# Kernel optimization log

Measured on AMD Instinct MI355X. Metric: run time of the kernel, lower is better.

## Reference

```python
import jax, jax.numpy as jnp
from jax import lax
import numpy as np

N, F_IN, D_MODEL = 8192, 128, 256
D_INNER, D_STATE, D_CONV, DT_RANK = 512, 16, 4, 16  # expand=2, d_state=16, d_conv=4, dt_rank=ceil(256/16)
BN_EPS = 1e-5


def setup_inputs() -> dict:
    key = jax.random.key(0)
    ks = jax.random.split(key, 12)
    rn = lambda k, s, sc: jax.random.normal(k, s, jnp.float32) * sc
    x = rn(ks[0], (N, F_IN), 1.0)
    # normalized dense adjacency (row sums ~1)
    adj = jax.random.uniform(ks[1], (N, N), jnp.float32) * (2.0 / N)
    w_gcn = rn(ks[2], (F_IN, D_MODEL), 1.0 / np.sqrt(F_IN))
    b_gcn = rn(ks[3], (D_MODEL,), 0.02)
    bn_gamma = jnp.ones((D_MODEL,), jnp.float32)
    bn_beta = jnp.zeros((D_MODEL,), jnp.float32)
    w_in = rn(ks[4], (2 * D_INNER, D_MODEL), 1.0 / np.sqrt(D_MODEL))
    conv_w = rn(ks[5], (D_INNER, D_CONV), 1.0 / np.sqrt(D_CONV))
    conv_b = rn(ks[6], (D_INNER,), 0.02)
    w_xproj = rn(ks[7], (DT_RANK + 2 * D_STATE, D_INNER), 1.0 / np.sqrt(D_INNER))
    w_dt = rn(ks[8], (D_INNER, DT_RANK), 1.0 / np.sqrt(DT_RANK))
    b_dt = rn(ks[9], (D_INNER,), 0.1)
    A_log = jnp.log(jnp.broadcast_to(jnp.arange(1, D_STATE + 1, dtype=jnp.float32), (D_INNER, D_STATE)))
    D_skip = jnp.ones((D_INNER,), jnp.float32)
    w_out = rn(ks[10], (D_MODEL, D_INNER), 1.0 / np.sqrt(D_INNER))
    return dict(x=x, adj=adj, w_gcn=w_gcn, b_gcn=b_gcn, bn_gamma=bn_gamma, bn_beta=bn_beta,
                w_in=w_in, conv_w=conv_w, conv_b=conv_b, w_xproj=w_xproj, w_dt=w_dt,
                b_dt=b_dt, A_log=A_log, D_skip=D_skip, w_out=w_out)


def _forward(x, adj, w_gcn, b_gcn, bn_gamma, bn_beta, w_in, conv_w, conv_b,
             w_xproj, w_dt, b_dt, A_log, D_skip, w_out):
    # --- GCN layer: adj @ (x @ W) + b ---
    h = adj @ (x @ w_gcn) + b_gcn            # (N, D_MODEL)
    h = jax.nn.relu(h)
    # dropout: eval mode -> identity
    # --- BatchNorm1d (batch statistics, biased var, as torch training norm) ---
    mean = jnp.mean(h, axis=0)
    var = jnp.var(h, axis=0)
    h = (h - mean) * lax.rsqrt(var + BN_EPS) * bn_gamma + bn_beta  # (N, D_MODEL)

    # --- Mamba block, batch=1, seq_len=N ---
    xz = h @ w_in.T                          # (N, 2*D_INNER)
    xm, z = jnp.split(xz, 2, axis=-1)        # (N, D_INNER) each

    # causal depthwise conv1d (kernel D_CONV) + SiLU
    xp = jnp.pad(xm, ((D_CONV - 1, 0), (0, 0)))
    xc = conv_b + sum(xp[i:i + N] * conv_w[:, i] for i in range(D_CONV))  # (N, D_INNER)
    xc = jax.nn.silu(xc)

    # input-dependent SSM parameters
    x_dbl = xc @ w_xproj.T                   # (N, DT_RANK + 2*D_STATE)
    dt_r = x_dbl[:, :DT_RANK]
    B = x_dbl[:, DT_RANK:DT_RANK + D_STATE]  # (N, D_STATE)
    C = x_dbl[:, DT_RANK + D_STATE:]         # (N, D_STATE)
    dt = jax.nn.softplus(dt_r @ w_dt.T + b_dt)  # (N, D_INNER)

    A = -jnp.exp(A_log)                      # (D_INNER, D_STATE)
    deltaA = jnp.exp(dt[:, :, None] * A[None])                 # (N, D_INNER, D_STATE)
    deltaBu = dt[:, :, None] * B[:, None, :] * xc[:, :, None]  # (N, D_INNER, D_STATE)

    def step(hs, inp):
        dA, dBu, c = inp
        hs = dA * hs + dBu                   # (D_INNER, D_STATE)
        return hs, hs @ c                    # emit (D_INNER,)

    h0 = jnp.zeros((D_INNER, D_STATE), xc.dtype)
    _, ys = lax.scan(step, h0, (deltaA, deltaBu, C))  # ys: (N, D_INNER)

    y = ys + D_skip * xc
    y = y * jax.nn.silu(z)
    out_m = y @ w_out.T                      # (N, D_MODEL)
    return out_m + h                         # residual


def reference(x, adj, w_gcn, b_gcn, bn_gamma, bn_beta, w_in, conv_w, conv_b,
              w_xproj, w_dt, b_dt, A_log, D_skip, w_out):
    return _forward(x, adj, w_gcn, b_gcn, bn_gamma, bn_beta, w_in, conv_w, conv_b,
                    w_xproj, w_dt, b_dt, A_log, D_skip, w_out)
```

## Files before the change

kernel.cpp:

```cpp
#include <hip/hip_runtime.h>
#include <stdint.h>

#define NN   8192
#define FIN  128
#define DM   256
#define DI   512
#define DST  16
#define NC   256
#define CL   32

typedef short bf16x8 __attribute__((ext_vector_type(8)));
typedef float f32x4 __attribute__((ext_vector_type(4)));
union FragU { unsigned u[4]; uint4 u4; bf16x8 v; };

__device__ __forceinline__ unsigned short f2bf(float x){
  unsigned u = __float_as_uint(x);
  return (unsigned short)((u + 0x7FFFu + ((u >> 16) & 1u)) >> 16);
}
__device__ __forceinline__ unsigned pack2(float a, float b){
  return (unsigned)f2bf(a) | ((unsigned)f2bf(b) << 16);
}
__device__ __forceinline__ unsigned pack2rn(float a, float b){
  unsigned ua = __float_as_uint(a) + 0x8000u;
  unsigned ub = __float_as_uint(b) + 0x8000u;
  return __builtin_amdgcn_perm(ub, ua, 0x07060302u);
}
__device__ __forceinline__ float bf2f(unsigned short u){
  return __uint_as_float(((unsigned)u) << 16);
}
__device__ __forceinline__ float sigmoidf_(float x){ return 1.f / (1.f + __expf(-x)); }
__device__ __forceinline__ f32x4 zero4(){ f32x4 z; z[0]=0.f; z[1]=0.f; z[2]=0.f; z[3]=0.f; return z; }

#define ASYNC16(g, l) __builtin_amdgcn_global_load_lds( \
    (const __attribute__((address_space(1))) void*)(g), \
    (__attribute__((address_space(3))) void*)(l), 16, 0, 0)
#define WAITVM10 asm volatile("s_waitcnt vmcnt(10)" ::: "memory")
#define WAITVM0  asm volatile("s_waitcnt vmcnt(0)" ::: "memory")
#define WAITLGKM0 asm volatile("s_waitcnt lgkmcnt(0)" ::: "memory")
#define BARRIER  asm volatile("s_barrier" ::: "memory")

constexpr size_t OFF_XWT   = 0;
constexpr size_t OFF_HB    = OFF_XWT   + (size_t)DM*NN*2;
constexpr size_t OFF_HBNB  = OFF_HB    + (size_t)NN*DM*2;
constexpr size_t OFF_WINB  = OFF_HBNB  + (size_t)NN*DM*2;
constexpr size_t OFF_WXPB  = OFF_WINB  + (size_t)1024*256*2;
constexpr size_t OFF_WOUTB = OFF_WXPB  + (size_t)48*512*2;
constexpr size_t OFF_XMB   = OFF_WOUTB + (size_t)256*512*2;
constexpr size_t OFF_ZB    = OFF_XMB   + (size_t)NN*DI*2;
constexpr size_t OFF_XCB   = OFF_ZB    + (size_t)NN*DI*2;
constexpr size_t OFF_XDBL  = OFF_XCB   + (size_t)NN*DI*2;
constexpr size_t OFF_DT    = OFF_XDBL  + (size_t)NN*48*4;
constexpr size_t OFF_PF    = OFF_DT    + (size_t)NN*DI*4;
constexpr size_t OFF_CY    = OFF_PF    + (size_t)NC*DI*DST*8;
constexpr size_t OFF_YB    = OFF_CY    + (size_t)NC*DI*DST*4;
constexpr size_t OFF_BNS   = OFF_YB    + (size_t)NN*DI*2;
constexpr size_t OFF_BNS2  = OFF_BNS   + 256*4;
constexpr size_t WS_NEED   = OFF_BNS2  + 256*4;
constexpr size_t OFF_HP    = OFF_PF;

__global__ __launch_bounds__(256) void prep_kernel(
    const float* __restrict__ w_in, const float* __restrict__ w_xp, const float* __restrict__ w_out,
    unsigned short* __restrict__ o_in, unsigned short* __restrict__ o_xp, unsigned short* __restrict__ o_out)
{
  int i = blockIdx.x * 256 + threadIdx.x;
  if (i < 1024*256) o_in[i]  = f2bf(w_in[i]);
  if (i < 48*512)   o_xp[i]  = f2bf(w_xp[i]);
  if (i < 256*512)  o_out[i] = f2bf(w_out[i]);
}

__global__ __launch_bounds__(256) void gemm1_kernel(
    const float* __restrict__ x, const float* __restrict__ w, unsigned short* __restrict__ xwT)
{
  __shared__ float xs[16*128];
  const int t = threadIdx.x;
  const int m0 = blockIdx.x * 16;
  {
    int r = t >> 4, c0 = (t & 15) * 8;
    const float* src = x + (size_t)(m0 + r)*FIN + c0;
    *(float4*)&xs[r*128 + c0]     = *(const float4*)src;
    *(float4*)&xs[r*128 + c0 + 4] = *(const float4*)(src + 4);
  }
  __syncthreads();
  const int n = t;
  float acc[16];
  #pragma unroll
  for (int m = 0; m < 16; ++m) acc[m] = 0.f;
  for (int k = 0; k < 128; k += 4){
    float w0 = w[(size_t)k*DM + n];
    float w1 = w[(size_t)(k+1)*DM + n];
    float w2 = w[(size_t)(k+2)*DM + n];
    float w3 = w[(size_t)(k+3)*DM + n];
    #pragma unroll
    for (int m = 0; m < 16; ++m){
      float4 xv = *(const float4*)&xs[m*128 + k];
      acc[m] = fmaf(xv.x, w0, acc[m]);
      acc[m] = fmaf(xv.y, w1, acc[m]);
      acc[m] = fmaf(xv.z, w2, acc[m]);
      acc[m] = fmaf(xv.w, w3, acc[m]);
    }
  }
  unsigned outp[8];
  #pragma unroll
  for (int m = 0; m < 8; ++m) outp[m] = pack2(acc[2*m], acc[2*m+1]);
  unsigned short* dst = xwT + (size_t)n*NN + m0;
  ((uint4*)dst)[0] = *(uint4*)&outp[0];
  ((uint4*)dst)[1] = *(uint4*)&outp[4];
}

__global__ __launch_bounds__(256, 2) void gemm2_kernel(
    const float* __restrict__ adj, const unsigned short* __restrict__ xwT,
    float* __restrict__ hp)
{
  extern __shared__ char lds[];
  const int t = threadIdx.x;
  const int wave = t >> 6, lane = t & 63, r = lane & 15, q = lane >> 4;
  const int mt = (int)blockIdx.x >> 2, ks = (int)blockIdx.x & 3;
  const int m0 = mt * 32;
  const int kb = ks * 2048;

  const float* asrc[2];
  #pragma unroll
  for (int j = 0; j < 2; ++j){
    int si = t + 256*j;
    int row = si >> 4, d = si & 15;
    int g = (d - 3*row) & 15;
    asrc[j] = adj + (size_t)(m0 + row)*NN + kb + g*4;
  }
  const unsigned short* bsrc[8];
  #pragma unroll
  for (int j = 0; j < 8; ++j){
    int si = t + 256*j;
    int n = si >> 3, d = si & 7;
    int g = (d - 3*n) & 7;
    bsrc[j] = xwT + (size_t)n*NN + kb + g*8;
  }

  f32x4 acc[2][4];
  #pragma unroll
  for (int mi = 0; mi < 2; ++mi)
    #pragma unroll
    for (int ni = 0; ni < 4; ++ni) acc[mi][ni] = zero4();

  #pragma unroll
  for (int s = 0; s < 2; ++s){
    char* L = lds + s*40960;
    int k0 = s*64;
    ASYNC16(asrc[0] + k0, L + t*16);
    ASYNC16(asrc[1] + k0, L + (t + 256)*16);
    #pragma unroll
    for (int j = 0; j < 8; ++j)
      ASYNC16(bsrc[j] + k0, L + 8192 + (t + 256*j)*16);
  }

  int aoffF[2][2][2];
  int boffU[2][4];
  #pragma unroll
  for (int ks2 = 0; ks2 < 2; ++ks2){
    #pragma unroll
    for (int mi = 0; mi < 2; ++mi){
      int m = mi*16 + r;
      int g0 = ks2*8 + 2*q;
      aoffF[ks2][mi][0] = m*64 + (((g0    ) + 3*m) & 15)*4;
      aoffF[ks2][mi][1] = m*64 + (((g0 + 1) + 3*m) & 15)*4;
    }
    #pragma unroll
    for (int ni = 0; ni < 4; ++ni){
      int n = wave*64 + ni*16 + r;
      int g = ks2*4 + q;
      boffU[ks2][ni] = 512 + n*8 + ((g + 3*n) & 7);
    }
  }

  for (int k = 0; k < 32; ++k){
    if (k < 31) { WAITVM10; } else { WAITVM0; }
    BARRIER;
    char* Lb = lds + (k & 1)*40960;
    const float* Af = (const float*)Lb;
    const uint4* Bu = (const uint4*)Lb;
    float4 pa[2][2][2];
    FragU fb[2][4];
    #pragma unroll
    for (int ks2 = 0; ks2 < 2; ++ks2){
      #pragma unroll
      for (int mi = 0; mi < 2; ++mi){
        pa[ks2][mi][0] = *(const float4*)(Af + aoffF[ks2][mi][0]);
        pa[ks2][mi][1] = *(const float4*)(Af + aoffF[ks2][mi][1]);
      }
      #pragma unroll
      for (int ni = 0; ni < 4; ++ni) fb[ks2][ni].u4 = Bu[boffU[ks2][ni]];
    }
    WAITLGKM0;
    BARRIER;
    if (k < 30){
      int k0 = (k + 2) * 64;
      ASYNC16(asrc[0] + k0, Lb + t*16);
      ASYNC16(asrc[1] + k0, Lb + (t + 256)*16);
      #pragma unroll
      for (int j = 0; j < 8; ++j)
        ASYNC16(bsrc[j] + k0, Lb + 8192 + (t + 256*j)*16);
    }
    FragU fa[2][2];
    #pragma unroll
    for (int ks2 = 0; ks2 < 2; ++ks2)
      #pragma unroll
      for (int mi = 0; mi < 2; ++mi){
        fa[ks2][mi].u[0] = pack2rn(pa[ks2][mi][0].x, pa[ks2][mi][0].y);
        fa[ks2][mi].u[1] = pack2rn(pa[ks2][mi][0].z, pa[ks2][mi][0].w);
        fa[ks2][mi].u[2] = pack2rn(pa[ks2][mi][1].x, pa[ks2][mi][1].y);
        fa[ks2][mi].u[3] = pack2rn(pa[ks2][mi][1].z, pa[ks2][mi][1].w);
      }
    #pragma unroll
    for (int ks2 = 0; ks2 < 2; ++ks2)
      #pragma unroll
      for (int mi = 0; mi < 2; ++mi)
        #pragma unroll
        for (int ni = 0; ni < 4; ++ni)
          acc[mi][ni] = __builtin_amdgcn_mfma_f32_16x16x32_bf16(fa[ks2][mi].v, fb[ks2][ni].v, acc[mi][ni], 0, 0, 0);
  }

  float* hpo = hp + (size_t)ks * ((size_t)NN * DM);
  #pragma unroll
  for (int mi = 0; mi < 2; ++mi)
    #pragma unroll
    for (int ni = 0; ni < 4; ++ni){
      const int n = wave*64 + ni*16 + r;
      #pragma unroll
      for (int jr = 0; jr < 4; ++jr){
        const int m = m0 + mi*16 + q*4 + jr;
        hpo[(size_t)m*DM + n] = acc[mi][ni][jr];
      }
    }
}

__global__ __launch_bounds__(256) void hred_kernel(
    const float* __restrict__ hp, const float* __restrict__ b_gcn,
    unsigned short* __restrict__ hb, float* __restrict__ bns, float* __restrict__ bns2)
{
  const size_t NND = (size_t)NN * DM;
  const int c = threadIdx.x;
  const int m0 = blockIdx.x * 32;
  const float bias = b_gcn[c];
  float s1 = 0.f, s2 = 0.f;
  #pragma unroll 8
  for (int rr = 0; rr < 32; ++rr){
    size_t idx = (size_t)(m0 + rr)*DM + c;
    float v = hp[idx] + hp[NND + idx] + hp[2*NND + idx] + hp[3*NND + idx] + bias;
    v = fmaxf(v, 0.f);
    hb[idx] = f2bf(v);
    s1 += v; s2 += v*v;
  }
  atomicAdd(bns + c, s1);
  atomicAdd(bns2 + c, s2);
}

__global__ __launch_bounds__(256) void bnapply_kernel(
    const unsigned short* __restrict__ hb, const float* __restrict__ s1, const float* __restrict__ s2,
    const float* __restrict__ gamma, const float* __restrict__ beta,
    unsigned short* __restrict__ hbnb)
{
  int base = (blockIdx.x*256 + threadIdx.x) * 2;
  int c0 = base & (DM - 1);
  ushort2 hv = *(const ushort2*)(hb + base);
  float mA = s1[c0] * (1.f/NN),   mB = s1[c0+1] * (1.f/NN);
  float vA = s2[c0] * (1.f/NN) - mA*mA, vB = s2[c0+1] * (1.f/NN) - mB*mB;
  float iA = rsqrtf(vA + 1e-5f), iB = rsqrtf(vB + 1e-5f);
  float a = (bf2f(hv.x) - mA)*iA*gamma[c0]   + beta[c0];
  float b = (bf2f(hv.y) - mB)*iB*gamma[c0+1] + beta[c0+1];
  ushort2 o; o.x = f2bf(a); o.y = f2bf(b);
  *(ushort2*)(hbnb + base) = o;
}

__global__ __launch_bounds__(256) void gemm3_kernel(
    const unsigned short* __restrict__ Ab, const unsigned short* __restrict__ Wb,
    unsigned short* __restrict__ xmb, unsigned short* __restrict__ zb)
{
  __shared__ uint4 alds[2048];
  const int t = threadIdx.x;
  const int wave = t >> 6, lane = t & 63, r = lane & 15, q = lane >> 4;
  const int mb = ((int)blockIdx.x & 127) * 64;
  const int nb = ((int)blockIdx.x >> 7) * 128;
  const int wm = wave & 1, wn = wave >> 1;

  #pragma unroll
  for (int j = 0; j < 8; ++j){
    int si = j*256 + t;
    int row = si >> 5, dg = si & 31;
    int sg = dg ^ (row & 31);
    ASYNC16(Ab + (size_t)(mb + row)*DM + sg*8, (char*)alds + si*16);
  }
  __syncthreads();

  f32x4 acc[2][4];
  #pragma unroll
  for (int mi = 0; mi < 2; ++mi)
    #pragma unroll
    for (int ni = 0; ni < 4; ++ni) acc[mi][ni] = zero4();

  const unsigned short* bp[4];
  #pragma unroll
  for (int ni = 0; ni < 4; ++ni)
    bp[ni] = Wb + (size_t)(nb + wn*64 + ni*16 + r)*DM + q*8;
  FragU fb[4];
  #pragma unroll
  for (int ni = 0; ni < 4; ++ni) fb[ni].u4 = *(const uint4*)bp[ni];

  #pragma unroll
  for (int it = 0; it < 8; ++it){
    FragU fbn[4];
    if (it < 7){
      #pragma unroll
      for (int ni = 0; ni < 4; ++ni) fbn[ni].u4 = *(const uint4*)(bp[ni] + (it+1)*32);
    }
    FragU fa[2];
    #pragma unroll
    for (int mi = 0; mi < 2; ++mi){
      int row = wm*32 + mi*16 + r;
      int g = it*4 + q;
      fa[mi].u4 = alds[row*32 + (g ^ (row & 31))];
    }
    #pragma unroll
    for (int mi = 0; mi < 2; ++mi)
      #pragma unroll
      for (int ni = 0; ni < 4; ++ni)
        acc[mi][ni] = __builtin_amdgcn_mfma_f32_16x16x32_bf16(fa[mi].v, fb[ni].v, acc[mi][ni], 0, 0, 0);
    if (it < 7){
      #pragma unroll
      for (int ni = 0; ni < 4; ++ni) fb[ni] = fbn[ni];
    }
  }
  #pragma unroll
  for (int mi = 0; mi < 2; ++mi)
    #pragma unroll
    for (int ni = 0; ni < 4; ++ni){
      int nc = nb + wn*64 + ni*16 + r;
      unsigned short* dst = (nc < 512) ? (xmb + nc) : (zb + (nc - 512));
      #pragma unroll
      for (int jr = 0; jr < 4; ++jr){
        int m = mb + wm*32 + mi*16 + q*4 + jr;
        dst[(size_t)m*DI] = f2bf(acc[mi][ni][jr]);
      }
    }
}

__global__ __launch_bounds__(256) void conv_kernel(
    const unsigned short* __restrict__ xmb, const float* __restrict__ conv_w, const float* __restrict__ conv_b,
    unsigned short* __restrict__ xcb)
{
  const int d0 = threadIdx.x * 2;
  const int n0 = blockIdx.x * 32;
  float4 wa = *(const float4*)(conv_w + (size_t)d0*4);
  float4 wb = *(const float4*)(conv_w + (size_t)d0*4 + 4);
  float2 bias = *(const float2*)(conv_b + d0);
  float x0a=0.f,x1a=0.f,x2a=0.f, x0b=0.f,x1b=0.f,x2b=0.f;
  #pragma unroll
  for (int j = 0; j < 3; ++j){
    int n = n0 - 3 + j;
    float va = 0.f, vb = 0.f;
    if (n >= 0){
      ushort2 u = *(const ushort2*)(xmb + (size_t)n*DI + d0);
      va = bf2f(u.x); vb = bf2f(u.y);
    }
    if (j == 0){ x0a = va; x0b = vb; }
    else if (j == 1){ x1a = va; x1b = vb; }
    else { x2a = va; x2b = vb; }
  }
  for (int j = 0; j < 32; ++j){
    int n = n0 + j;
    ushort2 u = *(const ushort2*)(xmb + (size_t)n*DI + d0);
    float x3a = bf2f(u.x), x3b = bf2f(u.y);
    float sa = bias.x + wa.x*x0a + wa.y*x1a + wa.z*x2a + wa.w*x3a;
    float sb = bias.y + wb.x*x0b + wb.y*x1b + wb.z*x2b + wb.w*x3b;
    float va = sa * sigmoidf_(sa);
    float vb = sb * sigmoidf_(sb);
    ushort2 o; o.x = f2bf(va); o.y = f2bf(vb);
    *(ushort2*)(xcb + (size_t)n*DI + d0) = o;
    x0a=x1a; x1a=x2a; x2a=x3a;
    x0b=x1b; x1b=x2b; x2b=x3b;
  }
}

__global__ __launch_bounds__(256) void gemm4_kernel(
    const unsigned short* __restrict__ Ab, const unsigned short* __restrict__ Wb, float* __restrict__ xdbl)
{
  __shared__ uint4 alds[2048];
  const int t = threadIdx.x;
  const int wave = t >> 6, lane = t & 63, r = lane & 15, q = lane >> 4;
  const int m0 = (int)blockIdx.x * 32;
  #pragma unroll
  for (int j = 0; j < 8; ++j){
    int si = j*256 + t;
    int row = si >> 6, dg = si & 63;
    int sg = dg ^ (row & 31);
    ASYNC16(Ab + (size_t)(m0 + row)*DI + sg*8, (char*)alds + si*16);
  }
  __syncthreads();
  f32x4 acc[2][3];
  #pragma unroll
  for (int mi = 0; mi < 2; ++mi)
    #pragma unroll
    for (int ni = 0; ni < 3; ++ni) acc[mi][ni] = zero4();
  const int kq = wave * 128;
  const unsigned short* bp[3];
  #pragma unroll
  for (int ni = 0; ni < 3; ++ni) bp[ni] = Wb + (size_t)(ni*16 + r)*DI + kq + q*8;
  FragU fb[3];
  #pragma unroll
  for (int ni = 0; ni < 3; ++ni) fb[ni].u4 = *(const uint4*)bp[ni];
  #pragma unroll
  for (int it = 0; it < 4; ++it){
    FragU fbn[3];
    if (it < 3){
      #pragma unroll
      for (int ni = 0; ni < 3; ++ni) fbn[ni].u4 = *(const uint4*)(bp[ni] + (it+1)*32);
    }
    FragU fa[2];
    #pragma unroll
    for (int mi = 0; mi < 2; ++mi){
      int row = mi*16 + r;
      int g = (kq >> 3) + it*4 + q;
      fa[mi].u4 = alds[row*64 + (g ^ (row & 31))];
    }
    #pragma unroll
    for (int mi = 0; mi < 2; ++mi)
      #pragma unroll
      for (int ni = 0; ni < 3; ++ni)
        acc[mi][ni] = __builtin_amdgcn_mfma_f32_16x16x32_bf16(fa[mi].v, fb[ni].v, acc[mi][ni], 0, 0, 0);
    if (it < 3){
      #pragma unroll
      for (int ni = 0; ni < 3; ++ni) fb[ni] = fbn[ni];
    }
  }
  __syncthreads();
  float* red = (float*)alds;
  if (wave > 0){
    int base = ((wave - 1)*64 + lane)*24;
    #pragma unroll
    for (int mi = 0; mi < 2; ++mi)
      #pragma unroll
      for (int ni = 0; ni < 3; ++ni)
        #pragma unroll
        for (int jr = 0; jr < 4; ++jr)
          red[base + (mi*3 + ni)*4 + jr] = acc[mi][ni][jr];
  }
  __syncthreads();
  if (wave == 0){
    #pragma unroll
    for (int w = 0; w < 3; ++w){
      int base = (w*64 + lane)*24;
      #pragma unroll
      for (int mi = 0; mi < 2; ++mi)
        #pragma unroll
        for (int ni = 0; ni < 3; ++ni)
          #pragma unroll
          for (int jr = 0; jr < 4; ++jr)
            acc[mi][ni][jr] += red[base + (mi*3 + ni)*4 + jr];
    }
    #pragma unroll
    for (int mi = 0; mi < 2; ++mi)
      #pragma unroll
      for (int ni = 0; ni < 3; ++ni)
        #pragma unroll
        for (int jr = 0; jr < 4; ++jr)
          xdbl[(size_t)(m0 + mi*16 + q*4 + jr)*48 + ni*16 + r] = acc[ni >= 0 ? mi : mi][ni][jr];
  }
}

__global__ __launch_bounds__(256) void dt_kernel(
    const float* __restrict__ xdbl, const float* __restrict__ w_dt, const float* __restrict__ b_dt,
    float* __restrict__ dt)
{
  __shared__ float xr[64*16];
  const int t = threadIdx.x;
  const int dg = (int)blockIdx.x & 1;
  const int n0 = ((int)blockIdx.x >> 1) * 64;
  const int d = dg*256 + t;
  #pragma unroll
  for (int j = 0; j < 4; ++j){
    int idx = t + 256*j;
    xr[idx] = xdbl[(size_t)(n0 + (idx >> 4))*48 + (idx & 15)];
  }
  __syncthreads();
  const float4* wp = (const float4*)(w_dt + (size_t)d*16);
  float4 w0 = wp[0], w1 = wp[1], w2 = wp[2], w3 = wp[3];
  float bias = b_dt[d];
  for (int j = 0; j < 64; ++j){
    const float4* xp = (const float4*)(xr + j*16);
    float4 a0 = xp[0], a1 = xp[1], a2 = xp[2], a3 = xp[3];
    float a = bias;
    a += w0.x*a0.x + w0.y*a0.y + w0.z*a0.z + w0.w*a0.w;
    a += w1.x*a1.x + w1.y*a1.y + w1.z*a1.z + w1.w*a1.w;
    a += w2.x*a2.x + w2.y*a2.y + w2.z*a2.z + w2.w*a2.w;
    a += w3.x*a3.x + w3.y*a3.y + w3.z*a3.z + w3.w*a3.w;
    float o = (a > 20.f) ? a : log1pf(__expf(a));
    dt[(size_t)(n0 + j)*DI + d] = o;
  }
}

__global__ __launch_bounds__(256) void scanA_kernel(
    const float* __restrict__ dt, const unsigned short* __restrict__ xcb,
    const float* __restrict__ xdbl, const float* __restrict__ A_log,
    float2* __restrict__ PF)
{
  __shared__ float Bs[CL*DST];
  const int t = threadIdx.x;
  const int c = (int)blockIdx.x >> 1;
  const int d = (((int)blockIdx.x & 1) << 8) + t;
  #pragma unroll
  for (int j = 0; j < 2; ++j){
    int idx = t + 256*j;
    Bs[idx] = xdbl[(size_t)(c*CL + (idx >> 4))*48 + 16 + (idx & 15)];
  }
  __syncthreads();
  float Av[DST], hs[DST];
  {
    const float4* Ap = (const float4*)(A_log + (size_t)d*DST);
    #pragma unroll
    for (int s4 = 0; s4 < 4; ++s4){
      float4 a4 = Ap[s4];
      Av[s4*4+0] = -__expf(a4.x); Av[s4*4+1] = -__expf(a4.y);
      Av[s4*4+2] = -__expf(a4.z); Av[s4*4+3] = -__expf(a4.w);
    }
  }
  #pragma unroll
  for (int s = 0; s < DST; ++s) hs[s] = 0.f;
  float sdt = 0.f;
  const size_t rb = (size_t)c*CL*DI + d;
  float dtv = dt[rb], xcv = bf2f(xcb[rb]);
  for (int tt = 0; tt < CL; ++tt){
    float dtn = 0.f, xcn = 0.f;
    if (tt + 1 < CL){
      dtn = dt[rb + (size_t)(tt+1)*DI];
      xcn = bf2f(xcb[rb + (size_t)(tt+1)*DI]);
    }
    float u = dtv * xcv;
    sdt += dtv;
    float bv[DST];
    *(float4*)&bv[0]  = *(const float4*)&Bs[tt*16];
    *(float4*)&bv[4]  = *(const float4*)&Bs[tt*16 + 4];
    *(float4*)&bv[8]  = *(const float4*)&Bs[tt*16 + 8];
    *(float4*)&bv[12] = *(const float4*)&Bs[tt*16 + 12];
    #pragma unroll
    for (int s = 0; s < DST; ++s)
      hs[s] = __expf(dtv * Av[s]) * hs[s] + u * bv[s];
    dtv = dtn; xcv = xcn;
  }
  float4* out = (float4*)(PF + (size_t)c*(DI*DST) + (size_t)d*DST);
  #pragma unroll
  for (int j = 0; j < 8; ++j){
    float4 v;
    v.x = __expf(Av[2*j] * sdt);   v.y = hs[2*j];
    v.z = __expf(Av[2*j+1] * sdt); v.w = hs[2*j+1];
    out[j] = v;
  }
}

__global__ __launch_bounds__(128) void scanB_kernel(
    const float2* __restrict__ PF, float* __restrict__ Cy)
{
  const int ds = (int)blockIdx.x*128 + (int)threadIdx.x;
  float2 A0[16], A1[16];
  #pragma unroll
  for (int j = 0; j < 16; ++j) A0[j] = PF[(size_t)j*8192 + ds];
  #pragma unroll
  for (int j = 0; j < 16; ++j) A1[j] = PF[(size_t)(16 + j)*8192 + ds];
  float cy = 0.f;
  Cy[ds] = 0.f;
  #pragma unroll
  for (int g = 0; g < 16; ++g){
    #pragma unroll
    for (int j = 0; j < 16; ++j){
      int i = g*16 + j;
      if (i < NC - 1){
        float2 pf = (g & 1) ? A1[j] : A0[j];
        cy = pf.x * cy + pf.y;
        Cy[(size_t)(i + 1)*8192 + ds] = cy;
      }
    }
    int gn = g + 2;
    if (gn < 16){
      #pragma unroll
      for (int j = 0; j < 16; ++j){
        float2 v = PF[(size_t)(gn*16 + j)*8192 + ds];
        if (g & 1) A1[j] = v; else A0[j] = v;
      }
    }
  }
}

__global__ __launch_bounds__(256) void scanC_kernel(
    const float* __restrict__ dt, const unsigned short* __restrict__ xcb,
    const float* __restrict__ xdbl, const float* __restrict__ A_log,
    const float* __restrict__ Cy, const float* __restrict__ Dskip,
    const unsigned short* __restrict__ zb, unsigned short* __restrict__ yb)
{
  __shared__ float Bs[CL*DST];
  __shared__ float Cs[CL*DST];
  const int t = threadIdx.x;
  const int c = (int)blockIdx.x >> 1;
  const int d = (((int)blockIdx.x & 1) << 8) + t;
  #pragma unroll
  for (int j = 0; j < 2; ++j){
    int idx = t + 256*j;
    int tg = c*CL + (idx >> 4);
    Bs[idx] = xdbl[(size_t)tg*48 + 16 + (idx & 15)];
    Cs[idx] = xdbl[(size_t)tg*48 + 32 + (idx & 15)];
  }
  __syncthreads();
  float Av[DST], hs[DST];
  {
    const float4* Ap = (const float4*)(A_log + (size_t)d*DST);
    #pragma unroll
    for (int s4 = 0; s4 < 4; ++s4){
      float4 a4 = Ap[s4];
      Av[s4*4+0] = -__expf(a4.x); Av[s4*4+1] = -__expf(a4.y);
      Av[s4*4+2] = -__expf(a4.z); Av[s4*4+3] = -__expf(a4.w);
    }
  }
  {
    const float4* hp4 = (const float4*)(Cy + (size_t)c*(DI*DST) + (size_t)d*DST);
    #pragma unroll
    for (int s4 = 0; s4 < 4; ++s4){
      float4 h4 = hp4[s4];
      hs[s4*4+0] = h4.x; hs[s4*4+1] = h4.y; hs[s4*4+2] = h4.z; hs[s4*4+3] = h4.w;
    }
  }
  const float Dv = Dskip[d];
  const size_t rb = (size_t)c*CL*DI + d;
  float dtv = dt[rb], xcv = bf2f(xcb[rb]);
  unsigned short zv0 = zb[rb];
  for (int tt = 0; tt < CL; ++tt){
    float dtn = 0.f, xcn = 0.f;
    unsigned short zn = 0;
    if (tt + 1 < CL){
      dtn = dt[rb + (size_t)(tt+1)*DI];
      xcn = bf2f(xcb[rb + (size_t)(tt+1)*DI]);
      zn  = zb[rb + (size_t)(tt+1)*DI];
    }
    float u = dtv * xcv;
    float bv[DST], cv[DST];
    *(float4*)&bv[0]  = *(const float4*)&Bs[tt*16];
    *(float4*)&bv[4]  = *(const float4*)&Bs[tt*16 + 4];
    *(float4*)&bv[8]  = *(const float4*)&Bs[tt*16 + 8];
    *(float4*)&bv[12] = *(const float4*)&Bs[tt*16 + 12];
    *(float4*)&cv[0]  = *(const float4*)&Cs[tt*16];
    *(float4*)&cv[4]  = *(const float4*)&Cs[tt*16 + 4];
    *(float4*)&cv[8]  = *(const float4*)&Cs[tt*16 + 8];
    *(float4*)&cv[12] = *(const float4*)&Cs[tt*16 + 12];
    float y0 = 0.f, y1 = 0.f;
    #pragma unroll
    for (int s = 0; s < DST; s += 2){
      hs[s]   = __expf(dtv * Av[s])   * hs[s]   + u * bv[s];
      hs[s+1] = __expf(dtv * Av[s+1]) * hs[s+1] + u * bv[s+1];
      y0 += hs[s]   * cv[s];
      y1 += hs[s+1] * cv[s+1];
    }
    float z = bf2f(zv0);
    float yf = ((y0 + y1) + Dv * xcv) * (z * sigmoidf_(z));
    yb[rb + (size_t)tt*DI] = f2bf(yf);
    dtv = dtn; xcv = xcn; zv0 = zn;
  }
}

__global__ __launch_bounds__(512) void gemm5_kernel(
    const unsigned short* __restrict__ yb, const unsigned short* __restrict__ Wb,
    const unsigned short* __restrict__ hbnb, float* __restrict__ out)
{
  __shared__ uint4 alds[2048];
  const int t = threadIdx.x;
  const int wave = t >> 6, lane = t & 63, r = lane & 15, q = lane >> 4;
  const int m0 = (int)blockIdx.x * 32;
  #pragma unroll
  for (int j = 0; j < 4; ++j){
    int si = j*512 + t;
    int row = si >> 6, dg = si & 63;
    int sg = dg ^ (row & 31);
    ASYNC16(yb + (size_t)(m0 + row)*DI + sg*8, (char*)alds + si*16);
  }
  __syncthreads();
  f32x4 acc[2][2];
  #pragma unroll
  for (int mi = 0; mi < 2; ++mi)
    #pragma unroll
    for (int ni = 0; ni < 2; ++ni) acc[mi][ni] = zero4();
  const int nw = wave * 32;
  const unsigned short* bp0 = Wb + (size_t)(nw + r)*DI + q*8;
  const unsigned short* bp1 = Wb + (size_t)(nw + 16 + r)*DI + q*8;
  FragU fb0, fb1;
  fb0.u4 = *(const uint4*)bp0;
  fb1.u4 = *(const uint4*)bp1;
  #pragma unroll
  for (int it = 0; it < 16; ++it){
    FragU fn0, fn1;
    if (it < 15){
      fn0.u4 = *(const uint4*)(bp0 + (it+1)*32);
      fn1.u4 = *(const uint4*)(bp1 + (it+1)*32);
    }
    FragU fa[2];
    #pragma unroll
    for (int mi = 0; mi < 2; ++mi){
      int row = mi*16 + r;
      int g = it*4 + q;
      fa[mi].u4 = alds[row*64 + (g ^ (row & 31))];
    }
    acc[0][0] = __builtin_amdgcn_mfma_f32_16x16x32_bf16(fa[0].v, fb0.v, acc[0][0], 0, 0, 0);
    acc[0][1] = __builtin_amdgcn_mfma_f32_16x16x32_bf16(fa[0].v, fb1.v, acc[0][1], 0, 0, 0);
    acc[1][0] = __builtin_amdgcn_mfma_f32_16x16x32_bf16(fa[1].v, fb0.v, acc[1][0], 0, 0, 0);
    acc[1][1] = __builtin_amdgcn_mfma_f32_16x16x32_bf16(fa[1].v, fb1.v, acc[1][1], 0, 0, 0);
    if (it < 15){ fb0 = fn0; fb1 = fn1; }
  }
  #pragma unroll
  for (int mi = 0; mi < 2; ++mi)
    #pragma unroll
    for (int ni = 0; ni < 2; ++ni){
      const int n = nw + ni*16 + r;
      #pragma unroll
      for (int jr = 0; jr < 4; ++jr){
        const int m = m0 + mi*16 + q*4 + jr;
        size_t idx = (size_t)m*DM + n;
        out[idx] = acc[mi][ni][jr] + bf2f(hbnb[idx]);
      }
    }
}

extern "C" void kernel_launch(void* const* d_in, const int* in_sizes, int n_in,
                              void* d_out, int out_size, void* d_ws, size_t ws_size,
                              hipStream_t stream)
{
  const float* x      = (const float*)d_in[0];
  const float* adj    = (const float*)d_in[1];
  const float* w_gcn  = (const float*)d_in[2];
  const float* b_gcn  = (const float*)d_in[3];
  const float* gamma  = (const float*)d_in[4];
  const float* beta   = (const float*)d_in[5];
  const float* w_in   = (const float*)d_in[6];
  const float* conv_w = (const float*)d_in[7];
  const float* conv_b = (const float*)d_in[8];
  const float* w_xp   = (const float*)d_in[9];
  const float* w_dt   = (const float*)d_in[10];
  const float* b_dt   = (const float*)d_in[11];
  const float* A_log  = (const float*)d_in[12];
  const float* D_skip = (const float*)d_in[13];
  const float* w_out  = (const float*)d_in[14];
  float* out = (float*)d_out;
  char* ws = (char*)d_ws;
  if (ws_size < WS_NEED) return;

  unsigned short* xwT   = (unsigned short*)(ws + OFF_XWT);
  float*          hp    = (float*)(ws + OFF_HP);
  unsigned short* hb    = (unsigned short*)(ws + OFF_HB);
  unsigned short* hbnb  = (unsigned short*)(ws + OFF_HBNB);
  unsigned short* winb  = (unsigned short*)(ws + OFF_WINB);
  unsigned short* wxpb  = (unsigned short*)(ws + OFF_WXPB);
  unsigned short* woutb = (unsigned short*)(ws + OFF_WOUTB);
  unsigned short* xmb   = (unsigned short*)(ws + OFF_XMB);
  unsigned short* zb    = (unsigned short*)(ws + OFF_ZB);
  unsigned short* xcb   = (unsigned short*)(ws + OFF_XCB);
  float*          xdbl  = (float*)(ws + OFF_XDBL);
  float*          dtb   = (float*)(ws + OFF_DT);
  float2*         PF    = (float2*)(ws + OFF_PF);
  float*          Cy    = (float*)(ws + OFF_CY);
  unsigned short* yb    = (unsigned short*)(ws + OFF_YB);
  float*          bns   = (float*)(ws + OFF_BNS);
  float*          bns2  = (float*)(ws + OFF_BNS2);

  hipMemsetAsync(bns, 0, 2*256*sizeof(float), stream);

  hipFuncSetAttribute((const void*)gemm2_kernel,
                      hipFuncAttributeMaxDynamicSharedMemorySize, 81920);

  prep_kernel   <<<1024, 256, 0, stream>>>(w_in, w_xp, w_out, winb, wxpb, woutb);
  gemm1_kernel  <<<512,  256, 0, stream>>>(x, w_gcn, xwT);
  gemm2_kernel  <<<1024, 256, 81920, stream>>>(adj, xwT, hp);
  hred_kernel   <<<256,  256, 0, stream>>>(hp, b_gcn, hb, bns, bns2);
  bnapply_kernel<<<4096, 256, 0, stream>>>(hb, bns, bns2, gamma, beta, hbnb);
  gemm3_kernel  <<<1024, 256, 0, stream>>>(hbnb, winb, xmb, zb);
  conv_kernel   <<<256,  256, 0, stream>>>(xmb, conv_w, conv_b, xcb);
  gemm4_kernel  <<<256,  256, 0, stream>>>(xcb, wxpb, xdbl);
  dt_kernel     <<<256,  256, 0, stream>>>(xdbl, w_dt, b_dt, dtb);
  scanA_kernel  <<<512,  256, 0, stream>>>(dtb, xcb, xdbl, A_log, PF);
  scanB_kernel  <<<64,   128, 0, stream>>>(PF, Cy);
  scanC_kernel  <<<512,  256, 0, stream>>>(dtb, xcb, xdbl, A_log, Cy, D_skip, zb, yb);
  gemm5_kernel  <<<256,  512, 0, stream>>>(yb, woutb, hbnb, out);
}
```

Measured before the change: 601.9 us.

## Retile adjacency GEMM with register prefetch, bf16 LDS, and fuse dt into gemm4

The adj@XW GEMM moves to 512-thread blocks with 64-row tiles and a 2-way K split instead of 32-row tiles and a 4-way split. That halves the partial-sum traffic that hred has to reduce. A tiles are now loaded into registers, converted to bf16 once, and written to a swizzled LDS layout, replacing async fp32 global-to-LDS copies that every wave had to convert itself. The dt projection plus softplus is fused into the gemm4 epilogue, which removes one kernel launch and a reread of xdbl. The risks are lower occupancy, since there is one 512-thread block per CU with only 256 blocks, and loads that no longer run asynchronously into LDS.

New measurement: 719.3 us. +19.5%, slower.

```diff
diff --git a/kernel.cpp b/kernel.cpp
--- a/kernel.cpp
+++ b/kernel.cpp
@@ -25,6 +25,12 @@
   unsigned ub = __float_as_uint(b) + 0x8000u;
   return __builtin_amdgcn_perm(ub, ua, 0x07060302u);
 }
+__device__ __forceinline__ uint4 packA8(float4 a, float4 b){
+  uint4 w;
+  w.x = pack2rn(a.x, a.y); w.y = pack2rn(a.z, a.w);
+  w.z = pack2rn(b.x, b.y); w.w = pack2rn(b.z, b.w);
+  return w;
+}
 __device__ __forceinline__ float bf2f(unsigned short u){
   return __uint_as_float(((unsigned)u) << 16);
 }
@@ -34,8 +40,6 @@
 #define ASYNC16(g, l) __builtin_amdgcn_global_load_lds( \
     (const __attribute__((address_space(1))) void*)(g), \
     (__attribute__((address_space(3))) void*)(l), 16, 0, 0)
-#define WAITVM10 asm volatile("s_waitcnt vmcnt(10)" ::: "memory")
-#define WAITVM0  asm volatile("s_waitcnt vmcnt(0)" ::: "memory")
 #define WAITLGKM0 asm volatile("s_waitcnt lgkmcnt(0)" ::: "memory")
 #define BARRIER  asm volatile("s_barrier" ::: "memory")
 
@@ -107,32 +111,29 @@
   ((uint4*)dst)[1] = *(uint4*)&outp[4];
 }
 
-__global__ __launch_bounds__(256, 2) void gemm2_kernel(
+__global__ __launch_bounds__(512, 1) void gemm2_kernel(
     const float* __restrict__ adj, const unsigned short* __restrict__ xwT,
     float* __restrict__ hp)
 {
   extern __shared__ char lds[];
   const int t = threadIdx.x;
   const int wave = t >> 6, lane = t & 63, r = lane & 15, q = lane >> 4;
-  const int mt = (int)blockIdx.x >> 2, ks = (int)blockIdx.x & 3;
-  const int m0 = mt * 32;
-  const int kb = ks * 2048;
-
-  const float* asrc[2];
-  #pragma unroll
-  for (int j = 0; j < 2; ++j){
-    int si = t + 256*j;
-    int row = si >> 4, d = si & 15;
-    int g = (d - 3*row) & 15;
-    asrc[j] = adj + (size_t)(m0 + row)*NN + kb + g*4;
-  }
-  const unsigned short* bsrc[8];
-  #pragma unroll
-  for (int j = 0; j < 8; ++j){
-    int si = t + 256*j;
-    int n = si >> 3, d = si & 7;
-    int g = (d - 3*n) & 7;
-    bsrc[j] = xwT + (size_t)n*NN + kb + g*8;
+  const int wm = wave & 1, wn = wave >> 1;
+  const int mt = (int)blockIdx.x >> 1, ks = (int)blockIdx.x & 1;
+  const int m0 = mt * 64;
+  const int kb = ks * 4096;
+
+  const int arow = t >> 3, aseg = t & 7;
+  const float* asrc = adj + (size_t)(m0 + arow)*NN + kb + aseg*8;
+  const int awOff = (arow*32 + ((aseg + arow) & 7)*4) * 4;
+  const unsigned short* bsrc[4];
+  int bwOff[4];
+  #pragma unroll
+  for (int j = 0; j < 4; ++j){
+    int si = t + 512*j;
+    int bn = si >> 3, bc = si & 7;
+    bsrc[j]  = xwT + (size_t)bn*NN + kb + bc*8;
+    bwOff[j] = 8192 + (bn*32 + ((bc + bn) & 7)*4) * 4;
   }
 
   f32x4 acc[2][4];
@@ -141,74 +142,63 @@
     #pragma unroll
     for (int ni = 0; ni < 4; ++ni) acc[mi][ni] = zero4();
 
-  #pragma unroll
-  for (int s = 0; s < 2; ++s){
-    char* L = lds + s*40960;
-    int k0 = s*64;
-    ASYNC16(asrc[0] + k0, L + t*16);
-    ASYNC16(asrc[1] + k0, L + (t + 256)*16);
-    #pragma unroll
-    for (int j = 0; j < 8; ++j)
-      ASYNC16(bsrc[j] + k0, L + 8192 + (t + 256*j)*16);
-  }
-
-  int aoffF[2][2][2];
-  int boffU[2][4];
+  int aro[2][2], bro[2][4];
   #pragma unroll
   for (int ks2 = 0; ks2 < 2; ++ks2){
+    int g = ks2*4 + q;
     #pragma unroll
     for (int mi = 0; mi < 2; ++mi){
-      int m = mi*16 + r;
-      int g0 = ks2*8 + 2*q;
-      aoffF[ks2][mi][0] = m*64 + (((g0    ) + 3*m) & 15)*4;
-      aoffF[ks2][mi][1] = m*64 + (((g0 + 1) + 3*m) & 15)*4;
+      int m = wm*32 + mi*16 + r;
+      aro[ks2][mi] = (m*32 + ((g + m) & 7)*4) * 4;
     }
     #pragma unroll
     for (int ni = 0; ni < 4; ++ni){
-      int n = wave*64 + ni*16 + r;
-      int g = ks2*4 + q;
-      boffU[ks2][ni] = 512 + n*8 + ((g + 3*n) & 7);
-    }
-  }
-
-  for (int k = 0; k < 32; ++k){
-    if (k < 31) { WAITVM10; } else { WAITVM0; }
-    BARRIER;
+      int n = wn*64 + ni*16 + r;
+      bro[ks2][ni] = 8192 + (n*32 + ((g + n) & 7)*4) * 4;
+    }
+  }
+
+  float4 arA[2], arB[2];
+  uint4  brr[2][4];
+
+  arA[0] = *(const float4*)(asrc);
+  arB[0] = *(const float4*)(asrc + 4);
+  #pragma unroll
+  for (int j = 0; j < 4; ++j) brr[0][j] = *(const uint4*)(bsrc[j]);
+  arA[1] = *(const float4*)(asrc + 64);
+  arB[1] = *(const float4*)(asrc + 68);
+  #pragma unroll
+  for (int j = 0; j < 4; ++j) brr[1][j] = *(const uint4*)(bsrc[j] + 64);
+  *(uint4*)(lds + awOff) = packA8(arA[0], arB[0]);
+  #pragma unroll
+  for (int j = 0; j < 4; ++j) *(uint4*)(lds + bwOff[j]) = brr[0][j];
+  WAITLGKM0; BARRIER;
+
+  #pragma unroll 2
+  for (int k = 0; k < 64; ++k){
     char* Lb = lds + (k & 1)*40960;
-    const float* Af = (const float*)Lb;
-    const uint4* Bu = (const uint4*)Lb;
-    float4 pa[2][2][2];
-    FragU fb[2][4];
+    FragU fa[2][2], fb[2][4];
     #pragma unroll
     for (int ks2 = 0; ks2 < 2; ++ks2){
       #pragma unroll
-      for (int mi = 0; mi < 2; ++mi){
-        pa[ks2][mi][0] = *(const float4*)(Af + aoffF[ks2][mi][0]);
-        pa[ks2][mi][1] = *(const float4*)(Af + aoffF[ks2][mi][1]);
-      }
-      #pragma unroll
-      for (int ni = 0; ni < 4; ++ni) fb[ks2][ni].u4 = Bu[boffU[ks2][ni]];
-    }
-    WAITLGKM0;
-    BARRIER;
-    if (k < 30){
-      int k0 = (k + 2) * 64;
-      ASYNC16(asrc[0] + k0, Lb + t*16);
-      ASYNC16(asrc[1] + k0, Lb + (t + 256)*16);
-      #pragma unroll
-      for (int j = 0; j < 8; ++j)
-        ASYNC16(bsrc[j] + k0, Lb + 8192 + (t + 256*j)*16);
-    }
-    FragU fa[2][2];
-    #pragma unroll
-    for (int ks2 = 0; ks2 < 2; ++ks2)
-      #pragma unroll
-      for (int mi = 0; mi < 2; ++mi){
-        fa[ks2][mi].u[0] = pack2rn(pa[ks2][mi][0].x, pa[ks2][mi][0].y);
-        fa[ks2][mi].u[1] = pack2rn(pa[ks2][mi][0].z, pa[ks2][mi][0].w);
-        fa[ks2][mi].u[2] = pack2rn(pa[ks2][mi][1].x, pa[ks2][mi][1].y);
-        fa[ks2][mi].u[3] = pack2rn(pa[ks2][mi][1].z, pa[ks2][mi][1].w);
-      }
+      for (int mi = 0; mi < 2; ++mi) fa[ks2][mi].u4 = *(const uint4*)(Lb + aro[ks2][mi]);
+      #pragma unroll
+      for (int ni = 0; ni < 4; ++ni) fb[ks2][ni].u4 = *(const uint4*)(Lb + bro[ks2][ni]);
+    }
+    if (k + 2 < 64){
+      int off = (k + 2) * 64;
+      arA[k & 1] = *(const float4*)(asrc + off);
+      arB[k & 1] = *(const float4*)(asrc + off + 4);
+      #pragma unroll
+      for (int j = 0; j < 4; ++j) brr[k & 1][j] = *(const uint4*)(bsrc[j] + off);
+    }
+    if (k + 1 < 64){
+      char* Lw = lds + ((k + 1) & 1)*40960;
+      const int b = (k + 1) & 1;
+      *(uint4*)(Lw + awOff) = packA8(arA[b], arB[b]);
+      #pragma unroll
+      for (int j = 0; j < 4; ++j) *(uint4*)(Lw + bwOff[j]) = brr[b][j];
+    }
     #pragma unroll
     for (int ks2 = 0; ks2 < 2; ++ks2)
       #pragma unroll
@@ -216,6 +206,7 @@
         #pragma unroll
         for (int ni = 0; ni < 4; ++ni)
           acc[mi][ni] = __builtin_amdgcn_mfma_f32_16x16x32_bf16(fa[ks2][mi].v, fb[ks2][ni].v, acc[mi][ni], 0, 0, 0);
+    WAITLGKM0; BARRIER;
   }
 
   float* hpo = hp + (size_t)ks * ((size_t)NN * DM);
@@ -223,10 +214,10 @@
   for (int mi = 0; mi < 2; ++mi)
     #pragma unroll
     for (int ni = 0; ni < 4; ++ni){
-      const int n = wave*64 + ni*16 + r;
+      const int n = wn*64 + ni*16 + r;
       #pragma unroll
       for (int jr = 0; jr < 4; ++jr){
-        const int m = m0 + mi*16 + q*4 + jr;
+        const int m = m0 + wm*32 + mi*16 + q*4 + jr;
         hpo[(size_t)m*DM + n] = acc[mi][ni][jr];
       }
     }
@@ -244,7 +235,7 @@
   #pragma unroll 8
   for (int rr = 0; rr < 32; ++rr){
     size_t idx = (size_t)(m0 + rr)*DM + c;
-    float v = hp[idx] + hp[NND + idx] + hp[2*NND + idx] + hp[3*NND + idx] + bias;
+    float v = hp[idx] + hp[NND + idx] + bias;
     v = fmaxf(v, 0.f);
     hb[idx] = f2bf(v);
     s1 += v; s2 += v*v;
@@ -380,9 +371,12 @@
 }
 
 __global__ __launch_bounds__(256) void gemm4_kernel(
-    const unsigned short* __restrict__ Ab, const unsigned short* __restrict__ Wb, float* __restrict__ xdbl)
+    const unsigned short* __restrict__ Ab, const unsigned short* __restrict__ Wb,
+    const float* __restrict__ w_dt, const float* __restrict__ b_dt,
+    float* __restrict__ xdbl, float* __restrict__ dt)
 {
   __shared__ uint4 alds[2048];
+  __shared__ float xr2[32*16];
   const int t = threadIdx.x;
   const int wave = t >> 6, lane = t & 63, r = lane & 15, q = lane >> 4;
   const int m0 = (int)blockIdx.x * 32;
@@ -461,38 +455,35 @@
       for (int ni = 0; ni < 3; ++ni)
         #pragma unroll
         for (int jr = 0; jr < 4; ++jr)
-          xdbl[(size_t)(m0 + mi*16 + q*4 + jr)*48 + ni*16 + r] = acc[ni >= 0 ? mi : mi][ni][jr];
-  }
-}
-
-__global__ __launch_bounds__(256) void dt_kernel(
-    const float* __restrict__ xdbl, const float* __restrict__ w_dt, const float* __restrict__ b_dt,
-    float* __restrict__ dt)
-{
-  __shared__ float xr[64*16];
-  const int t = threadIdx.x;
-  const int dg = (int)blockIdx.x & 1;
-  const int n0 = ((int)blockIdx.x >> 1) * 64;
-  const int d = dg*256 + t;
-  #pragma unroll
-  for (int j = 0; j < 4; ++j){
-    int idx = t + 256*j;
-    xr[idx] = xdbl[(size_t)(n0 + (idx >> 4))*48 + (idx & 15)];
-  }
-  __syncthreads();
-  const float4* wp = (const float4*)(w_dt + (size_t)d*16);
-  float4 w0 = wp[0], w1 = wp[1], w2 = wp[2], w3 = wp[3];
-  float bias = b_dt[d];
-  for (int j = 0; j < 64; ++j){
-    const float4* xp = (const float4*)(xr + j*16);
+          xdbl[(size_t)(m0 + mi*16 + q*4 + jr)*48 + ni*16 + r] = acc[mi][ni][jr];
+    #pragma unroll
+    for (int mi = 0; mi < 2; ++mi)
+      #pragma unroll
+      for (int jr = 0; jr < 4; ++jr)
+        xr2[(mi*16 + q*4 + jr)*16 + r] = acc[mi][0][jr];
+  }
+  __syncthreads();
+  const int d0 = t * 2;
+  const float4* wp0 = (const float4*)(w_dt + (size_t)d0*16);
+  const float4* wp1 = (const float4*)(w_dt + (size_t)(d0+1)*16);
+  float4 wA0 = wp0[0], wA1 = wp0[1], wA2 = wp0[2], wA3 = wp0[3];
+  float4 wB0 = wp1[0], wB1 = wp1[1], wB2 = wp1[2], wB3 = wp1[3];
+  float2 bb = *(const float2*)(b_dt + d0);
+  for (int j = 0; j < 32; ++j){
+    const float4* xp = (const float4*)(xr2 + j*16);
     float4 a0 = xp[0], a1 = xp[1], a2 = xp[2], a3 = xp[3];
-    float a = bias;
-    a += w0.x*a0.x + w0.y*a0.y + w0.z*a0.z + w0.w*a0.w;
-    a += w1.x*a1.x + w1.y*a1.y + w1.z*a1.z + w1.w*a1.w;
-    a += w2.x*a2.x + w2.y*a2.y + w2.z*a2.z + w2.w*a2.w;
-    a += w3.x*a3.x + w3.y*a3.y + w3.z*a3.z + w3.w*a3.w;
-    float o = (a > 20.f) ? a : log1pf(__expf(a));
-    dt[(size_t)(n0 + j)*DI + d] = o;
+    float sA = bb.x, sB = bb.y;
+    sA += wA0.x*a0.x + wA0.y*a0.y + wA0.z*a0.z + wA0.w*a0.w;
+    sA += wA1.x*a1.x + wA1.y*a1.y + wA1.z*a1.z + wA1.w*a1.w;
+    sA += wA2.x*a2.x + wA2.y*a2.y + wA2.z*a2.z + wA2.w*a2.w;
+    sA += wA3.x*a3.x + wA3.y*a3.y + wA3.z*a3.z + wA3.w*a3.w;
+    sB += wB0.x*a0.x + wB0.y*a0.y + wB0.z*a0.z + wB0.w*a0.w;
+    sB += wB1.x*a1.x + wB1.y*a1.y + wB1.z*a1.z + wB1.w*a1.w;
+    sB += wB2.x*a2.x + wB2.y*a2.y + wB2.z*a2.z + wB2.w*a2.w;
+    sB += wB3.x*a3.x + wB3.y*a3.y + wB3.z*a3.z + wB3.w*a3.w;
+    float oA = (sA > 20.f) ? sA : log1pf(__expf(sA));
+    float oB = (sB > 20.f) ? sB : log1pf(__expf(sB));
+    *(float2*)(dt + (size_t)(m0 + j)*DI + d0) = make_float2(oA, oB);
   }
 }
 
@@ -770,13 +761,12 @@
 
   prep_kernel   <<<1024, 256, 0, stream>>>(w_in, w_xp, w_out, winb, wxpb, woutb);
   gemm1_kernel  <<<512,  256, 0, stream>>>(x, w_gcn, xwT);
-  gemm2_kernel  <<<1024, 256, 81920, stream>>>(adj, xwT, hp);
+  gemm2_kernel  <<<256,  512, 81920, stream>>>(adj, xwT, hp);
   hred_kernel   <<<256,  256, 0, stream>>>(hp, b_gcn, hb, bns, bns2);
   bnapply_kernel<<<4096, 256, 0, stream>>>(hb, bns, bns2, gamma, beta, hbnb);
   gemm3_kernel  <<<1024, 256, 0, stream>>>(hbnb, winb, xmb, zb);
   conv_kernel   <<<256,  256, 0, stream>>>(xmb, conv_w, conv_b, xcb);
-  gemm4_kernel  <<<256,  256, 0, stream>>>(xcb, wxpb, xdbl);
-  dt_kernel     <<<256,  256, 0, stream>>>(xdbl, w_dt, b_dt, dtb);
+  gemm4_kernel  <<<256,  256, 0, stream>>>(xcb, wxpb, w_dt, b_dt, xdbl, dtb);
   scanA_kernel  <<<512,  256, 0, stream>>>(dtb, xcb, xdbl, A_log, PF);
   scanB_kernel  <<<64,   128, 0, stream>>>(PF, Cy);
   scanC_kernel  <<<512,  256, 0, stream>>>(dtb, xcb, xdbl, A_log, Cy, D_skip, zb, yb);
```
